# Optimization experiments

Hardware: AMD Instinct MI355X
Metric: run time of the kernel (lower is better)

The kernel has to match this reference:

```python
import jax, jax.numpy as jnp
import numpy as np

DIM = 384
HEADS = 8
EPS = 1e-5


def _layernorm(x, g, b):
    mu = jnp.mean(x, axis=-1, keepdims=True)
    var = jnp.mean(jnp.square(x - mu), axis=-1, keepdims=True)
    return (x - mu) * jax.lax.rsqrt(var + EPS) * g + b


def setup_inputs() -> dict:
    key = jax.random.key(0)
    ks = jax.random.split(key, 16)
    d = DIM
    s = lambda k, shape, scale=0.02: jax.random.normal(k, shape, dtype=jnp.float32) * scale
    return {
        "x": jax.random.normal(ks[0], (16, d, 32, 32), dtype=jnp.float32),
        "pos_w": s(ks[1], (d, 1, 3, 3), 0.1),   # depthwise conv kernel (OIHW, I=1)
        "pos_b": jnp.zeros((d,), jnp.float32),
        "g1": jnp.ones((d,), jnp.float32),
        "b1": jnp.zeros((d,), jnp.float32),
        "wqkv": s(ks[2], (d, 3 * d)),
        "bqkv": jnp.zeros((3 * d,), jnp.float32),
        "wproj": s(ks[3], (d, d)),
        "bproj": jnp.zeros((d,), jnp.float32),
        "g2": jnp.ones((d,), jnp.float32),
        "b2": jnp.zeros((d,), jnp.float32),
        "w1": s(ks[4], (d, 4 * d)),
        "bf1": jnp.zeros((4 * d,), jnp.float32),
        "w2": s(ks[5], (4 * d, d)),
        "bf2": jnp.zeros((d,), jnp.float32),
    }


def reference(x, pos_w, pos_b, g1, b1, wqkv, bqkv, wproj, bproj, g2, b2, w1, bf1, w2, bf2):
    B, C, H, W = x.shape
    # depthwise 3x3 conv positional embedding, residual
    pe = jax.lax.conv_general_dilated(
        x, pos_w, window_strides=(1, 1), padding=((1, 1), (1, 1)),
        dimension_numbers=("NCHW", "OIHW", "NCHW"), feature_group_count=C)
    x = x + pe + pos_b[None, :, None, None]
    # to tokens [B, N, C]
    t = x.reshape(B, C, H * W).transpose(0, 2, 1)
    N = H * W
    Dh = C // HEADS
    # attention
    xn = _layernorm(t, g1, b1)
    qkv = xn @ wqkv + bqkv                                   # [B,N,3C]
    qkv = qkv.reshape(B, N, 3, HEADS, Dh)
    q, k, v = qkv[:, :, 0], qkv[:, :, 1], qkv[:, :, 2]        # [B,N,H,Dh]
    scale = Dh ** -0.5
    attn = jnp.einsum("bqhd,bkhd->bhqk", q, k) * scale
    attn = jax.nn.softmax(attn, axis=-1)
    o = jnp.einsum("bhqk,bkhd->bqhd", attn, v).reshape(B, N, C)
    t = t + o @ wproj + bproj
    # MLP
    yn = _layernorm(t, g2, b2)
    h = jax.nn.gelu(yn @ w1 + bf1, approximate=False)
    t = t + h @ w2 + bf2
    return t.transpose(0, 2, 1).reshape(B, C, H, W)
```

## Files before the change

kernel.cpp:

```cpp
#include <hip/hip_runtime.h>
#include <hip/hip_bf16.h>
#include <math.h>

#define BATCH 16
#define CDIM 384
#define HH 32
#define WW 32
#define NPIX 1024
#define MTOK (BATCH * NPIX)
#define NHEADS 8
#define DH 48
#define QKVN (3 * CDIM)
#define FFN (4 * CDIM)

typedef unsigned short u16;
typedef unsigned int u32;
typedef __attribute__((ext_vector_type(8))) short short8;
typedef __attribute__((ext_vector_type(4))) float floatx4;

#define MFMA16(a, b, c) __builtin_amdgcn_mfma_f32_16x16x32_bf16(a, b, c, 0, 0, 0)

__device__ __forceinline__ void gl2lds16(const void* g, void* l) {
    __builtin_amdgcn_global_load_lds(
        (const __attribute__((address_space(1))) void*)g,
        (__attribute__((address_space(3))) void*)l, 16, 0, 0);
}

__device__ __forceinline__ u32 pkbf(float a, float b) {
    u32 ua = __float_as_uint(a) + 0x8000u;
    u32 ub = __float_as_uint(b) + 0x8000u;
    return __builtin_amdgcn_perm(ub, ua, 0x07060302u);
}
__device__ __forceinline__ float bf2f(u16 h) { return __uint_as_float(((u32)h) << 16); }
__device__ __forceinline__ u16 f2bf(float f) {
    u32 u = __float_as_uint(f);
    return (u16)((u + 0x7FFFu + ((u >> 16) & 1u)) >> 16);
}

__global__ __launch_bounds__(256) void conv_pe_kernel(const float* __restrict__ x,
                                                      const float* __restrict__ pos_w,
                                                      const float* __restrict__ pos_b,
                                                      float* __restrict__ t) {
    __shared__ float xs[64][100];
    __shared__ float os[32][68];
    const int cg = blockIdx.x, h = blockIdx.y, b = blockIdx.z;
    const int tid = threadIdx.x;
    const int c0 = cg * 64;

#pragma unroll
    for (int it = 0; it < 6; ++it) {
        int task = tid + it * 256;
        int c = task / 24, rem = task % 24;
        int row = rem >> 3, f4 = rem & 7;
        int hh = h + row - 1;
        float4 v = {0.f, 0.f, 0.f, 0.f};
        if (hh >= 0 && hh < HH)
            v = *(const float4*)(x + (((size_t)(b * CDIM + c0 + c) * HH + hh) * WW + f4 * 4));
        *(float4*)&xs[c][row * 32 + f4 * 4] = v;
    }
    __syncthreads();

    const int c = tid >> 2, w0 = (tid & 3) * 8;
    float wgt[9];
#pragma unroll
    for (int i = 0; i < 9; ++i) wgt[i] = pos_w[(c0 + c) * 9 + i];
    const float pb = pos_b[c0 + c];
#pragma unroll
    for (int wi = 0; wi < 8; ++wi) {
        int w = w0 + wi;
        float acc = 0.f;
#pragma unroll
        for (int r = 0; r < 3; ++r)
#pragma unroll
            for (int kw = 0; kw < 3; ++kw) {
                int w2 = w + kw - 1;
                if (w2 >= 0 && w2 < WW) acc += xs[c][r * 32 + w2] * wgt[r * 3 + kw];
            }
        os[w][c] = xs[c][32 + w] + acc + pb;
    }
    __syncthreads();

    float* dstb = t + (size_t)(b * NPIX + h * 32) * CDIM + c0;
#pragma unroll
    for (int it = 0; it < 2; ++it) {
        int task = tid + it * 256;
        int px = task >> 4, f4 = task & 15;
        *(float4*)(dstb + (size_t)px * CDIM + f4 * 4) = *(const float4*)&os[px][f4 * 4];
    }
}

__global__ void ln_kernel(const float* __restrict__ in,
                          const float* __restrict__ g,
                          const float* __restrict__ bta,
                          __hip_bfloat16* __restrict__ out) {
    int m = blockIdx.x;
    const float* row = in + (size_t)m * CDIM;
    int tid = threadIdx.x;
    float v0 = row[tid], v1 = row[tid + 128], v2 = row[tid + 256];
    float s = v0 + v1 + v2;
    float ss = v0 * v0 + v1 * v1 + v2 * v2;
#pragma unroll
    for (int off = 32; off > 0; off >>= 1) {
        s += __shfl_down(s, off, 64);
        ss += __shfl_down(ss, off, 64);
    }
    __shared__ float red[4];
    if ((tid & 63) == 0) { red[tid >> 6] = s; red[2 + (tid >> 6)] = ss; }
    __syncthreads();
    float sum = red[0] + red[1], sumsq = red[2] + red[3];
    float mu = sum * (1.f / CDIM);
    float var = sumsq * (1.f / CDIM) - mu * mu;
    float rstd = rsqrtf(var + 1e-5f);
    __hip_bfloat16* orow = out + (size_t)m * CDIM;
    orow[tid]       = __float2bfloat16((v0 - mu) * rstd * g[tid] + bta[tid]);
    orow[tid + 128] = __float2bfloat16((v1 - mu) * rstd * g[tid + 128] + bta[tid + 128]);
    orow[tid + 256] = __float2bfloat16((v2 - mu) * rstd * g[tid + 256] + bta[tid + 256]);
}

__global__ void wt_kernel(const float* __restrict__ W, __hip_bfloat16* __restrict__ Wt,
                          int K, int N) {
    __shared__ float tile[32][33];
    int n0 = blockIdx.x * 32, k0 = blockIdx.y * 32;
    int tx = threadIdx.x & 31, ty = threadIdx.x >> 5;
    for (int i = ty; i < 32; i += 8) tile[i][tx] = W[(size_t)(k0 + i) * N + n0 + tx];
    __syncthreads();
    for (int i = ty; i < 32; i += 8)
        Wt[(size_t)(n0 + i) * K + k0 + tx] = __float2bfloat16(tile[tx][i]);
}

__global__ __launch_bounds__(256) void vtrans_kernel(const u16* __restrict__ qkv,
                                                     u16* __restrict__ vT) {
    __shared__ u16 Vl[48][136];
    const int kt = blockIdx.x, h = blockIdx.y, b = blockIdx.z;
    const int tid = threadIdx.x;
    const size_t base = (size_t)b * NPIX * QKVN + 2 * CDIM + (size_t)h * DH;
#pragma unroll
    for (int it = 0; it < 3; ++it) {
        int task = tid + it * 256;
        int key = task / 6, ch = task - key * 6;
        short8 v = *(const short8*)(qkv + base + (size_t)(kt * 128 + key) * QKVN + ch * 8);
#pragma unroll
        for (int i = 0; i < 8; ++i) Vl[ch * 8 + i][key] = (u16)v[i];
    }
    __syncthreads();
    u16* dst = vT + (size_t)(b * NHEADS + h) * DH * NPIX + (size_t)kt * 128;
#pragma unroll
    for (int it = 0; it < 3; ++it) {
        int task = tid + it * 256;
        int d = task >> 4, ch = task & 15;
        short8 v = *(const short8*)&Vl[d][ch * 8];
        *(short8*)(dst + (size_t)d * NPIX + ch * 8) = v;
    }
}

template <int BN, int BK, int RES, int ACT, int OUTBF>
__global__ __launch_bounds__(256) void gemm_bf16(
    const u16* __restrict__ A, const u16* __restrict__ Bt,
    const float* __restrict__ bias, const float* __restrict__ Res,
    void* __restrict__ Cout, int N, int K) {
    constexpr int KC = BK / 32;
    constexpr int NF = BN / 32;
    __shared__ u16 As[2][KC][128 * 32];
    __shared__ u16 Bs[2][KC][BN * 32];
    const int tid = threadIdx.x;
    const int lane = tid & 63;
    const int wv = tid >> 6;
    const int qd = lane >> 4;
    const int l16 = lane & 15;
    const int wy = wv >> 1, wx = wv & 1;

    const int id = blockIdx.x;
    const int xcd = id & 7, j = id >> 3;
    const int m0 = (xcd * 16 + (j & 15)) * 128;
    const int n0 = (j >> 4) * BN;

    const int rr = tid >> 2, cc = (tid & 3) * 8;
    const u16* Ag = A + (size_t)(m0 + rr) * K + cc;
    const u16* Bg = Bt + (size_t)(n0 + rr) * K + cc;

    const floatx4 fz = {0.f, 0.f, 0.f, 0.f};
    floatx4 acc[4][NF];
#pragma unroll
    for (int i = 0; i < 4; ++i)
#pragma unroll
        for (int jj = 0; jj < NF; ++jj) acc[i][jj] = fz;

    auto stage = [&](int slot, int k0) {
#pragma unroll
        for (int kc = 0; kc < KC; ++kc) {
            gl2lds16(Ag + k0 + kc * 32, &As[slot][kc][0] + tid * 8);
            gl2lds16(Ag + (size_t)64 * K + k0 + kc * 32, &As[slot][kc][0] + 2048 + tid * 8);
            gl2lds16(Bg + k0 + kc * 32, &Bs[slot][kc][0] + tid * 8);
            if (NF == 4) gl2lds16(Bg + (size_t)64 * K + k0 + kc * 32, &Bs[slot][kc][0] + 2048 + tid * 8);
        }
    };

    stage(0, 0);
    const int iters = K / BK;
    for (int it = 0; it < iters; ++it) {
        const int slot = it & 1;
        __syncthreads();
        if (it + 1 < iters) stage(slot ^ 1, (it + 1) * BK);
#pragma unroll
        for (int kc = 0; kc < KC; ++kc) {
            short8 af[4], bfr[NF];
#pragma unroll
            for (int i = 0; i < 4; ++i)
                af[i] = *(const short8*)(&As[slot][kc][0] + (wy * 64 + i * 16 + l16) * 32 + qd * 8);
#pragma unroll
            for (int jj = 0; jj < NF; ++jj)
                bfr[jj] = *(const short8*)(&Bs[slot][kc][0] + (wx * (BN / 2) + jj * 16 + l16) * 32 + qd * 8);
#pragma unroll
            for (int i = 0; i < 4; ++i)
#pragma unroll
                for (int jj = 0; jj < NF; ++jj) acc[i][jj] = MFMA16(bfr[jj], af[i], acc[i][jj]);
        }
    }

    const int rowb = m0 + wy * 64 + l16;
    const int colb = n0 + wx * (BN / 2) + qd * 4;
#pragma unroll
    for (int jj = 0; jj < NF; ++jj) {
        int col = colb + jj * 16;
        float4 bb = *(const float4*)(bias + col);
#pragma unroll
        for (int i = 0; i < 4; ++i) {
            int row = rowb + i * 16;
            floatx4 a = acc[i][jj];
            float v0 = a[0] + bb.x, v1 = a[1] + bb.y, v2 = a[2] + bb.z, v3 = a[3] + bb.w;
            if (RES) {
                float4 rv = *(const float4*)(Res + (size_t)row * N + col);
                v0 += rv.x; v1 += rv.y; v2 += rv.z; v3 += rv.w;
            }
            if (ACT) {
                v0 = 0.5f * v0 * (1.f + erff(v0 * 0.70710678118654752f));
                v1 = 0.5f * v1 * (1.f + erff(v1 * 0.70710678118654752f));
                v2 = 0.5f * v2 * (1.f + erff(v2 * 0.70710678118654752f));
                v3 = 0.5f * v3 * (1.f + erff(v3 * 0.70710678118654752f));
            }
            if (OUTBF) {
                uint2 pk;
                pk.x = pkbf(v0, v1);
                pk.y = pkbf(v2, v3);
                *(uint2*)((__hip_bfloat16*)Cout + (size_t)row * N + col) = pk;
            } else {
                float4 st = {v0, v1, v2, v3};
                *(float4*)((float*)Cout + (size_t)row * N + col) = st;
            }
        }
    }
}

__global__ __launch_bounds__(256) void attn_kernel(const u16* __restrict__ qkv,
                                                   const u16* __restrict__ vT,
                                                   __hip_bfloat16* __restrict__ ob) {
    const int id = blockIdx.x;
    const int h = id & 7;
    const int b = (id >> 3) & 15;
    const int qb = id >> 7;
    const int tid = threadIdx.x;
    const int lane = tid & 63, wv = tid >> 6;
    const int qd = lane >> 4, l16 = lane & 15;

    __shared__ u16 Kl[2][65][48];
    __shared__ __align__(16) u16 Vt[48][72];
    __shared__ __align__(16) u16 Plt[4][16][72];

    if (tid < 24) { ((u32*)&Kl[0][64][0])[tid] = 0; ((u32*)&Kl[1][64][0])[tid] = 0; }

    const size_t bh = (size_t)b * NPIX * QKVN + (size_t)h * DH;
    const u16* vtb = vT + (size_t)(b * NHEADS + h) * DH * NPIX;

    auto stageK = [&](int kt, int slot) {
        const size_t kbase = bh + (size_t)(kt * 64) * QKVN + CDIM;
        int key = tid / 6, ch = tid - key * 6;
        gl2lds16(qkv + kbase + (size_t)key * QKVN + ch * 8, &Kl[slot][0][0] + tid * 8);
        if (tid < 128) {
            int t2 = tid + 256;
            int k2 = t2 / 6, c2 = t2 - k2 * 6;
            gl2lds16(qkv + kbase + (size_t)k2 * QKVN + c2 * 8, &Kl[slot][0][0] + t2 * 8);
        }
    };
    const int vd = tid >> 3, vc = tid & 7, vd1 = (tid + 256) >> 3;
    short8 vA, vB;
    auto loadV = [&](int kt) {
        vA = *(const short8*)(vtb + (size_t)vd * NPIX + kt * 64 + vc * 8);
        if (tid < 128) vB = *(const short8*)(vtb + (size_t)vd1 * NPIX + kt * 64 + vc * 8);
    };

    const float qsc = 0.14433756729740643f * 1.4426950408889634f;
    short8 qf[2][2];
    const short8 z8 = {0, 0, 0, 0, 0, 0, 0, 0};
#pragma unroll
    for (int g = 0; g < 2; ++g) {
        const u16* gq = qkv + bh + (size_t)(qb * 128 + wv * 32 + g * 16 + l16) * QKVN;
        short8 q0 = *(const short8*)(gq + qd * 8);
        short8 q1 = (qd < 2) ? *(const short8*)(gq + 32 + qd * 8) : z8;
#pragma unroll
        for (int e = 0; e < 8; ++e) {
            q0[e] = (short)f2bf(bf2f((u16)q0[e]) * qsc);
            q1[e] = (short)f2bf(bf2f((u16)q1[e]) * qsc);
        }
        qf[g][0] = q0;
        qf[g][1] = q1;
    }

    const floatx4 fz = {0.f, 0.f, 0.f, 0.f};
    floatx4 o[2][3];
    float lsum[2] = {0.f, 0.f};
#pragma unroll
    for (int g = 0; g < 2; ++g)
#pragma unroll
        for (int nt = 0; nt < 3; ++nt) o[g][nt] = fz;

    stageK(0, 0);
    loadV(0);

    for (int kt = 0; kt < 16; ++kt) {
        const int cur = kt & 1;
        __syncthreads();
        *(short8*)&Vt[vd][vc * 8] = vA;
        if (tid < 128) *(short8*)&Vt[vd1][vc * 8] = vB;
        __syncthreads();
        if (kt + 1 < 16) { stageK(kt + 1, cur ^ 1); loadV(kt + 1); }

        short8 kl[4], kh[4];
#pragma unroll
        for (int t = 0; t < 4; ++t) {
            const u16* kr = &Kl[cur][0][0] + (t * 16 + l16) * 48;
            kl[t] = *(const short8*)(kr + qd * 8);
            kh[t] = *(const short8*)(kr + 32 + qd * 8);
        }
        short8 vl[3], vh[3];
#pragma unroll
        for (int nt = 0; nt < 3; ++nt) {
            const u16* vr = &Vt[0][0] + (nt * 16 + l16) * 72;
            vl[nt] = *(const short8*)(vr + qd * 8);
            vh[nt] = *(const short8*)(vr + 32 + qd * 8);
        }

#pragma unroll
        for (int g = 0; g < 2; ++g) {
#pragma unroll
            for (int t = 0; t < 4; ++t) {
                floatx4 a = fz;
                a = MFMA16(kl[t], qf[g][0], a);
                a = MFMA16(kh[t], qf[g][1], a);
                float p0 = __builtin_amdgcn_exp2f(a[0]);
                float p1 = __builtin_amdgcn_exp2f(a[1]);
                float p2 = __builtin_amdgcn_exp2f(a[2]);
                float p3 = __builtin_amdgcn_exp2f(a[3]);
                lsum[g] += (p0 + p1) + (p2 + p3);
                uint2 w;
                w.x = pkbf(p0, p1);
                w.y = pkbf(p2, p3);
                *(uint2*)&Plt[wv][l16][t * 16 + qd * 4] = w;
            }
            short8 ap0 = *(const short8*)&Plt[wv][l16][qd * 8];
            short8 ap1 = *(const short8*)&Plt[wv][l16][32 + qd * 8];
#pragma unroll
            for (int nt = 0; nt < 3; ++nt) {
                o[g][nt] = MFMA16(vl[nt], ap0, o[g][nt]);
                o[g][nt] = MFMA16(vh[nt], ap1, o[g][nt]);
            }
        }
    }

#pragma unroll
    for (int g = 0; g < 2; ++g) {
        float l = lsum[g];
        l += __shfl_xor(l, 16, 64);
        l += __shfl_xor(l, 32, 64);
        float inv = 1.f / l;
        __hip_bfloat16* orow =
            ob + (size_t)(b * NPIX + qb * 128 + wv * 32 + g * 16 + l16) * CDIM + h * DH;
#pragma unroll
        for (int nt = 0; nt < 3; ++nt) {
            float v0 = o[g][nt][0] * inv, v1 = o[g][nt][1] * inv;
            float v2 = o[g][nt][2] * inv, v3 = o[g][nt][3] * inv;
            uint2 w;
            w.x = pkbf(v0, v1);
            w.y = pkbf(v2, v3);
            *(uint2*)(orow + nt * 16 + qd * 4) = w;
        }
    }
}

__global__ void transpose_kernel(const float* __restrict__ t, float* __restrict__ out) {
    __shared__ float tile[32][33];
    int b = blockIdx.z;
    int n0 = blockIdx.x * 32;
    int c0 = blockIdx.y * 32;
    int tx = threadIdx.x & 31;
    int ty = threadIdx.x >> 5;
    for (int i = ty; i < 32; i += 8)
        tile[i][tx] = t[(size_t)(b * NPIX + n0 + i) * CDIM + c0 + tx];
    __syncthreads();
    int c = threadIdx.x >> 3, f4 = threadIdx.x & 7;
    float4 v;
    v.x = tile[f4 * 4 + 0][c];
    v.y = tile[f4 * 4 + 1][c];
    v.z = tile[f4 * 4 + 2][c];
    v.w = tile[f4 * 4 + 3][c];
    *(float4*)(out + (size_t)(b * CDIM + c0 + c) * NPIX + n0 + f4 * 4) = v;
}

extern "C" void kernel_launch(void* const* d_in, const int* in_sizes, int n_in,
                              void* d_out, int out_size, void* d_ws, size_t ws_size,
                              hipStream_t stream) {
    const float* x = (const float*)d_in[0];
    const float* pos_w = (const float*)d_in[1];
    const float* pos_b = (const float*)d_in[2];
    const float* g1 = (const float*)d_in[3];
    const float* b1 = (const float*)d_in[4];
    const float* wqkv = (const float*)d_in[5];
    const float* bqkv = (const float*)d_in[6];
    const float* wproj = (const float*)d_in[7];
    const float* bproj = (const float*)d_in[8];
    const float* g2 = (const float*)d_in[9];
    const float* b2 = (const float*)d_in[10];
    const float* w1 = (const float*)d_in[11];
    const float* bf1 = (const float*)d_in[12];
    const float* w2 = (const float*)d_in[13];
    const float* bf2 = (const float*)d_in[14];
    float* out = (float*)d_out;

    char* ws = (char*)d_ws;
    float* t = (float*)ws;
    __hip_bfloat16* xn = (__hip_bfloat16*)(ws + 25165824);
    u16* vTb = (u16*)xn;
    __hip_bfloat16* wqkvT = (__hip_bfloat16*)(ws + 37748736);
    __hip_bfloat16* wprojT = (__hip_bfloat16*)(ws + 38633472);
    __hip_bfloat16* w1T = (__hip_bfloat16*)(ws + 38928384);
    __hip_bfloat16* w2T = (__hip_bfloat16*)(ws + 40108032);
    char* big = ws + 41287680;
    u16* qkvb = (u16*)big;
    __hip_bfloat16* obb = (__hip_bfloat16*)(big + 37748736);
    u16* hb = (u16*)big;

    wt_kernel<<<dim3(QKVN / 32, CDIM / 32), 256, 0, stream>>>(wqkv, wqkvT, CDIM, QKVN);
    wt_kernel<<<dim3(CDIM / 32, CDIM / 32), 256, 0, stream>>>(wproj, wprojT, CDIM, CDIM);
    wt_kernel<<<dim3(FFN / 32, CDIM / 32), 256, 0, stream>>>(w1, w1T, CDIM, FFN);
    wt_kernel<<<dim3(CDIM / 32, FFN / 32), 256, 0, stream>>>(w2, w2T, FFN, CDIM);

    conv_pe_kernel<<<dim3(CDIM / 64, HH, BATCH), 256, 0, stream>>>(x, pos_w, pos_b, t);
    ln_kernel<<<MTOK, 128, 0, stream>>>(t, g1, b1, xn);
    gemm_bf16<128, 32, 0, 0, 1><<<dim3(128 * (QKVN / 128)), 256, 0, stream>>>(
        (const u16*)xn, (const u16*)wqkvT, bqkv, nullptr, qkvb, QKVN, CDIM);
    vtrans_kernel<<<dim3(NPIX / 128, NHEADS, BATCH), 256, 0, stream>>>(qkvb, vTb);
    attn_kernel<<<dim3(1024), 256, 0, stream>>>(qkvb, vTb, obb);
    gemm_bf16<64, 64, 1, 0, 0><<<dim3(128 * (CDIM / 64)), 256, 0, stream>>>(
        (const u16*)obb, (const u16*)wprojT, bproj, t, t, CDIM, CDIM);
    ln_kernel<<<MTOK, 128, 0, stream>>>(t, g2, b2, xn);
    gemm_bf16<128, 32, 0, 1, 1><<<dim3(128 * (FFN / 128)), 256, 0, stream>>>(
        (const u16*)xn, (const u16*)w1T, bf1, nullptr, hb, FFN, CDIM);
    gemm_bf16<64, 64, 1, 0, 0><<<dim3(128 * (CDIM / 64)), 256, 0, stream>>>(
        (const u16*)hb, (const u16*)w2T, bf2, t, t, CDIM, FFN);
    transpose_kernel<<<dim3(32, 12, BATCH), 256, 0, stream>>>(t, out);
}
```

Measured before the change: 340.0 us.

## Fuse output transpose into FFN2 epilogue, async-stage swizzled V in attention, merge weight transposes

The final GEMM now writes straight into the NCHW output layout, which removes the separate transpose kernel and its round trip through memory. In attention, V tiles are double-buffered via global-to-LDS loads, using an XOR-swizzled layout written by vtrans; this drops the register staging step and one barrier per iteration. The four weight-transpose launches are merged into a single kernel. The strided scalar output stores may coalesce less well than the old float4 path.

```diff
diff --git a/kernel.cpp b/kernel.cpp
--- a/kernel.cpp
+++ b/kernel.cpp
@@ -117,10 +117,21 @@
     orow[tid + 256] = __float2bfloat16((v2 - mu) * rstd * g[tid + 256] + bta[tid + 256]);
 }
 
-__global__ void wt_kernel(const float* __restrict__ W, __hip_bfloat16* __restrict__ Wt,
-                          int K, int N) {
+__global__ void wt_all_kernel(const float* __restrict__ wqkv, const float* __restrict__ wproj,
+                              const float* __restrict__ w1, const float* __restrict__ w2,
+                              __hip_bfloat16* __restrict__ wqkvT, __hip_bfloat16* __restrict__ wprojT,
+                              __hip_bfloat16* __restrict__ w1T, __hip_bfloat16* __restrict__ w2T) {
     __shared__ float tile[32][33];
-    int n0 = blockIdx.x * 32, k0 = blockIdx.y * 32;
+    int id = blockIdx.x;
+    const float* W;
+    __hip_bfloat16* Wt;
+    int K, N, tidx;
+    if (id < 432)       { W = wqkv;  Wt = wqkvT;  K = 384;  N = 1152; tidx = id; }
+    else if (id < 576)  { W = wproj; Wt = wprojT; K = 384;  N = 384;  tidx = id - 432; }
+    else if (id < 1152) { W = w1;    Wt = w1T;    K = 384;  N = 1536; tidx = id - 576; }
+    else                { W = w2;    Wt = w2T;    K = 1536; N = 384;  tidx = id - 1152; }
+    int ntx = N / 32;
+    int n0 = (tidx % ntx) * 32, k0 = (tidx / ntx) * 32;
     int tx = threadIdx.x & 31, ty = threadIdx.x >> 5;
     for (int i = ty; i < 32; i += 8) tile[i][tx] = W[(size_t)(k0 + i) * N + n0 + tx];
     __syncthreads();
@@ -149,11 +160,12 @@
         int task = tid + it * 256;
         int d = task >> 4, ch = task & 15;
         short8 v = *(const short8*)&Vl[d][ch * 8];
-        *(short8*)(dst + (size_t)d * NPIX + ch * 8) = v;
-    }
-}
-
-template <int BN, int BK, int RES, int ACT, int OUTBF>
+        int pos = (ch & 7) ^ (d & 7);
+        *(short8*)(dst + (size_t)d * NPIX + (ch & 8) * 8 + pos * 8) = v;
+    }
+}
+
+template <int BN, int BK, int RES, int ACT, int OUTMODE>
 __global__ __launch_bounds__(256) void gemm_bf16(
     const u16* __restrict__ A, const u16* __restrict__ Bt,
     const float* __restrict__ bias, const float* __restrict__ Res,
@@ -238,14 +250,21 @@
                 v2 = 0.5f * v2 * (1.f + erff(v2 * 0.70710678118654752f));
                 v3 = 0.5f * v3 * (1.f + erff(v3 * 0.70710678118654752f));
             }
-            if (OUTBF) {
+            if (OUTMODE == 1) {
                 uint2 pk;
                 pk.x = pkbf(v0, v1);
                 pk.y = pkbf(v2, v3);
                 *(uint2*)((__hip_bfloat16*)Cout + (size_t)row * N + col) = pk;
-            } else {
+            } else if (OUTMODE == 0) {
                 float4 st = {v0, v1, v2, v3};
                 *(float4*)((float*)Cout + (size_t)row * N + col) = st;
+            } else {
+                int b_ = row >> 10, p = row & 1023;
+                float* op = (float*)Cout + ((size_t)(b_ * CDIM + col)) * NPIX + p;
+                op[0] = v0;
+                op[NPIX] = v1;
+                op[2 * NPIX] = v2;
+                op[3 * NPIX] = v3;
             }
         }
     }
@@ -262,11 +281,9 @@
     const int lane = tid & 63, wv = tid >> 6;
     const int qd = lane >> 4, l16 = lane & 15;
 
-    __shared__ u16 Kl[2][65][48];
-    __shared__ __align__(16) u16 Vt[48][72];
-    __shared__ __align__(16) u16 Plt[4][16][72];
-
-    if (tid < 24) { ((u32*)&Kl[0][64][0])[tid] = 0; ((u32*)&Kl[1][64][0])[tid] = 0; }
+    __shared__ u16 Kl[2][65 * 48];
+    __shared__ u16 Vt[2][48 * 64];
+    __shared__ __align__(16) u16 Plt[4][16 * 72];
 
     const size_t bh = (size_t)b * NPIX * QKVN + (size_t)h * DH;
     const u16* vtb = vT + (size_t)(b * NHEADS + h) * DH * NPIX;
@@ -274,18 +291,18 @@
     auto stageK = [&](int kt, int slot) {
         const size_t kbase = bh + (size_t)(kt * 64) * QKVN + CDIM;
         int key = tid / 6, ch = tid - key * 6;
-        gl2lds16(qkv + kbase + (size_t)key * QKVN + ch * 8, &Kl[slot][0][0] + tid * 8);
+        gl2lds16(qkv + kbase + (size_t)key * QKVN + ch * 8, &Kl[slot][0] + tid * 8);
         if (tid < 128) {
             int t2 = tid + 256;
             int k2 = t2 / 6, c2 = t2 - k2 * 6;
-            gl2lds16(qkv + kbase + (size_t)k2 * QKVN + c2 * 8, &Kl[slot][0][0] + t2 * 8);
+            gl2lds16(qkv + kbase + (size_t)k2 * QKVN + c2 * 8, &Kl[slot][0] + t2 * 8);
         }
     };
-    const int vd = tid >> 3, vc = tid & 7, vd1 = (tid + 256) >> 3;
-    short8 vA, vB;
-    auto loadV = [&](int kt) {
-        vA = *(const short8*)(vtb + (size_t)vd * NPIX + kt * 64 + vc * 8);
-        if (tid < 128) vB = *(const short8*)(vtb + (size_t)vd1 * NPIX + kt * 64 + vc * 8);
+    auto stageV = [&](int kt, int slot) {
+        const u16* vbase = vtb + (size_t)kt * 64 + (tid & 7) * 8;
+        gl2lds16(vbase + (size_t)(tid >> 3) * NPIX, &Vt[slot][0] + tid * 8);
+        if (tid < 128)
+            gl2lds16(vbase + (size_t)((tid + 256) >> 3) * NPIX, &Vt[slot][0] + (tid + 256) * 8);
     };
 
     const float qsc = 0.14433756729740643f * 1.4426950408889634f;
@@ -314,29 +331,27 @@
         for (int nt = 0; nt < 3; ++nt) o[g][nt] = fz;
 
     stageK(0, 0);
-    loadV(0);
+    stageV(0, 0);
+    const int sw = l16 & 7;
 
     for (int kt = 0; kt < 16; ++kt) {
         const int cur = kt & 1;
         __syncthreads();
-        *(short8*)&Vt[vd][vc * 8] = vA;
-        if (tid < 128) *(short8*)&Vt[vd1][vc * 8] = vB;
-        __syncthreads();
-        if (kt + 1 < 16) { stageK(kt + 1, cur ^ 1); loadV(kt + 1); }
+        if (kt + 1 < 16) { stageK(kt + 1, cur ^ 1); stageV(kt + 1, cur ^ 1); }
 
         short8 kl[4], kh[4];
 #pragma unroll
         for (int t = 0; t < 4; ++t) {
-            const u16* kr = &Kl[cur][0][0] + (t * 16 + l16) * 48;
+            const u16* kr = &Kl[cur][0] + (t * 16 + l16) * 48;
             kl[t] = *(const short8*)(kr + qd * 8);
             kh[t] = *(const short8*)(kr + 32 + qd * 8);
         }
         short8 vl[3], vh[3];
 #pragma unroll
         for (int nt = 0; nt < 3; ++nt) {
-            const u16* vr = &Vt[0][0] + (nt * 16 + l16) * 72;
-            vl[nt] = *(const short8*)(vr + qd * 8);
-            vh[nt] = *(const short8*)(vr + 32 + qd * 8);
+            const u16* vr = &Vt[cur][0] + (nt * 16 + l16) * 64;
+            vl[nt] = *(const short8*)(vr + (qd ^ sw) * 8);
+            vh[nt] = *(const short8*)(vr + ((qd + 4) ^ sw) * 8);
         }
 
 #pragma unroll
@@ -354,10 +369,10 @@
                 uint2 w;
                 w.x = pkbf(p0, p1);
                 w.y = pkbf(p2, p3);
-                *(uint2*)&Plt[wv][l16][t * 16 + qd * 4] = w;
-            }
-            short8 ap0 = *(const short8*)&Plt[wv][l16][qd * 8];
-            short8 ap1 = *(const short8*)&Plt[wv][l16][32 + qd * 8];
+                *(uint2*)&Plt[wv][l16 * 72 + t * 16 + qd * 4] = w;
+            }
+            short8 ap0 = *(const short8*)&Plt[wv][l16 * 72 + qd * 8];
+            short8 ap1 = *(const short8*)&Plt[wv][l16 * 72 + 32 + qd * 8];
 #pragma unroll
             for (int nt = 0; nt < 3; ++nt) {
                 o[g][nt] = MFMA16(vl[nt], ap0, o[g][nt]);
@@ -384,25 +399,6 @@
             *(uint2*)(orow + nt * 16 + qd * 4) = w;
         }
     }
-}
-
-__global__ void transpose_kernel(const float* __restrict__ t, float* __restrict__ out) {
-    __shared__ float tile[32][33];
-    int b = blockIdx.z;
-    int n0 = blockIdx.x * 32;
-    int c0 = blockIdx.y * 32;
-    int tx = threadIdx.x & 31;
-    int ty = threadIdx.x >> 5;
-    for (int i = ty; i < 32; i += 8)
-        tile[i][tx] = t[(size_t)(b * NPIX + n0 + i) * CDIM + c0 + tx];
-    __syncthreads();
-    int c = threadIdx.x >> 3, f4 = threadIdx.x & 7;
-    float4 v;
-    v.x = tile[f4 * 4 + 0][c];
-    v.y = tile[f4 * 4 + 1][c];
-    v.z = tile[f4 * 4 + 2][c];
-    v.w = tile[f4 * 4 + 3][c];
-    *(float4*)(out + (size_t)(b * CDIM + c0 + c) * NPIX + n0 + f4 * 4) = v;
 }
 
 extern "C" void kernel_launch(void* const* d_in, const int* in_sizes, int n_in,
@@ -438,11 +434,8 @@
     __hip_bfloat16* obb = (__hip_bfloat16*)(big + 37748736);
     u16* hb = (u16*)big;
 
-    wt_kernel<<<dim3(QKVN / 32, CDIM / 32), 256, 0, stream>>>(wqkv, wqkvT, CDIM, QKVN);
-    wt_kernel<<<dim3(CDIM / 32, CDIM / 32), 256, 0, stream>>>(wproj, wprojT, CDIM, CDIM);
-    wt_kernel<<<dim3(FFN / 32, CDIM / 32), 256, 0, stream>>>(w1, w1T, CDIM, FFN);
-    wt_kernel<<<dim3(CDIM / 32, FFN / 32), 256, 0, stream>>>(w2, w2T, FFN, CDIM);
-
+    wt_all_kernel<<<dim3(1728), 256, 0, stream>>>(wqkv, wproj, w1, w2,
+                                                  wqkvT, wprojT, w1T, w2T);
     conv_pe_kernel<<<dim3(CDIM / 64, HH, BATCH), 256, 0, stream>>>(x, pos_w, pos_b, t);
     ln_kernel<<<MTOK, 128, 0, stream>>>(t, g1, b1, xn);
     gemm_bf16<128, 32, 0, 0, 1><<<dim3(128 * (QKVN / 128)), 256, 0, stream>>>(
@@ -454,7 +447,6 @@
     ln_kernel<<<MTOK, 128, 0, stream>>>(t, g2, b2, xn);
     gemm_bf16<128, 32, 0, 1, 1><<<dim3(128 * (FFN / 128)), 256, 0, stream>>>(
         (const u16*)xn, (const u16*)w1T, bf1, nullptr, hb, FFN, CDIM);
-    gemm_bf16<64, 64, 1, 0, 0><<<dim3(128 * (CDIM / 64)), 256, 0, stream>>>(
-        (const u16*)hb, (const u16*)w2T, bf2, t, t, CDIM, FFN);
-    transpose_kernel<<<dim3(32, 12, BATCH), 256, 0, stream>>>(t, out);
-}
+    gemm_bf16<64, 64, 1, 0, 2><<<dim3(128 * (CDIM / 64)), 256, 0, stream>>>(
+        (const u16*)hb, (const u16*)w2T, bf2, t, out, CDIM, FFN);
+}
```

Result: faster. 319.4 us (-6.1%).
